# Kernel tuning notes

Hardware: AMD Instinct MI355X
Metric: run time of the kernel (lower is better)

## Reference

```python
import jax, jax.numpy as jnp
import numpy as np

HEAD_DIM = 16

def setup_inputs() -> dict:
    key = jax.random.key(0)
    ks = jax.random.split(key, 5)
    unif, h, d = 128, 8, 16
    batch, n = 4, 2048
    return {
        "Wq": jax.random.normal(ks[0], (unif, h, d), jnp.float32) * 0.05,
        "Wk": jax.random.normal(ks[1], (unif, h, d), jnp.float32) * 0.05,
        "Wv": jax.random.normal(ks[2], (unif, d, h), jnp.float32) * 0.05,
        "Wo": jax.random.normal(ks[3], (d, h, unif), jnp.float32) * 0.05,
        "vec": jax.random.normal(ks[4], (batch, n, unif), jnp.float32),
    }

def reference(Wq, Wk, Wv, Wo, vec):
    # projections: 'kij,abk->abij'
    qv = jnp.einsum('khd,bnk->bnhd', Wq, vec)          # [b,n,h,d]
    kv = jnp.einsum('khd,bnk->bnhd', Wk, vec)          # [b,n,h,d]
    vv = jnp.einsum('kdh,bnk->bndh', Wv, vec)          # [b,n,d,h]
    # full O(N^2) score tensor: 'aibk,ajbk->aijb'
    compat = jnp.einsum('bihd,bjhd->bijh', qv, kv) / np.sqrt(HEAD_DIM)  # [b,n,n,h]
    weight = jax.nn.softmax(compat, axis=2)
    # 'aijb,ajkb->aikb'
    received = jnp.einsum('bijh,bjdh->bidh', weight, vv)  # [b,n,d,h]
    # 'ijk,alij->alk'
    mha = jnp.einsum('dho,bndh->bno', Wo, received)       # [b,n,unif]
    return mha
```

## Files before the change

### kernel.cpp

```cpp
#include <hip/hip_runtime.h>
#include <hip/hip_bf16.h>

#define UNIF 128
#define NH   8
#define HD   16
#define BATCH 4
#define SEQ  2048
#define ROWS (BATCH*SEQ)

typedef __attribute__((ext_vector_type(8)))  short bf16x8;
typedef __attribute__((ext_vector_type(16))) float f32x16;
typedef __attribute__((ext_vector_type(4)))  float f32x4;
typedef __attribute__((ext_vector_type(4)))  unsigned uint32x4;
typedef __attribute__((ext_vector_type(2)))  unsigned uint2v;

static __device__ __forceinline__ unsigned f2bf(float x) {
    unsigned u = __builtin_bit_cast(unsigned, x);
    return (u + 0x7fffu + ((u >> 16) & 1u)) >> 16;
}
static __device__ __forceinline__ unsigned pkbf(float a, float b) {
    return f2bf(a) | (f2bf(b) << 16);
}
static __device__ __forceinline__ unsigned short bfs(float x) {
    return (unsigned short)f2bf(x);
}
static __device__ __forceinline__ unsigned cvtpk(float a, float b) {
    unsigned r;
    asm("v_cvt_pk_bf16_f32 %0, %1, %2" : "=v"(r) : "v"(a), "v"(b));
    return r;
}
static __device__ __forceinline__ void plswap(unsigned &a, unsigned &b) {
    uint2v r = __builtin_amdgcn_permlane32_swap(a, b, false, false);
    a = r[0]; b = r[1];
}
static __device__ __forceinline__ bf16x8 ld8f(const float* p) {
    const float4 x = *(const float4*)p;
    const float4 y = *(const float4*)(p + 4);
    uint32x4 u = { cvtpk(x.x, x.y), cvtpk(x.z, x.w),
                   cvtpk(y.x, y.y), cvtpk(y.z, y.w) };
    return __builtin_bit_cast(bf16x8, u);
}

__global__ __launch_bounds__(256) void prep_kernel(
    const float* __restrict__ Wq, const float* __restrict__ Wk,
    const float* __restrict__ Wv, const float* __restrict__ Wo,
    unsigned short* __restrict__ Wqt, unsigned short* __restrict__ Wkt,
    unsigned short* __restrict__ Wvt, unsigned short* __restrict__ Wot)
{
    const int m  = blockIdx.x >> 3;
    const int r0 = (blockIdx.x & 7) * 16;
    unsigned short* dst = (m==0)?Wqt:(m==1)?Wkt:(m==2)?Wvt:Wot;
    const float qsc = 0.25f * 1.4426950408889634f;
    for (int t = threadIdx.x; t < 16*UNIF; t += 256) {
        const int r = r0 + (t >> 7), s = t & 127;
        float val;
        if (m == 0)      val = Wq[s*UNIF + r] * qsc;
        else if (m == 1) val = Wk[s*UNIF + r];
        else if (m == 2) val = Wv[s*UNIF + (r & 15)*NH + (r >> 4)];
        else             val = Wo[((s & 15)*NH + (s >> 4))*UNIF + r];
        dst[r*UNIF + s] = bfs(val);
    }
}

__global__ __launch_bounds__(256) void proj_kernel(
    const float* __restrict__ vec,  const unsigned short* __restrict__ Wqt,
    const unsigned short* __restrict__ Wkt, const unsigned short* __restrict__ Wvt,
    unsigned short* __restrict__ Qbf, unsigned short* __restrict__ Kbf,
    unsigned short* __restrict__ Vt)
{
    const int sel  = blockIdx.y;
    const int row0 = blockIdx.x * 32;
    const int b    = row0 >> 11;
    const int n0   = row0 & (SEQ-1);
    const int lane = threadIdx.x & 63;
    const int w    = threadIdx.x >> 6;
    const int l15  = lane & 15, g = lane >> 4;
    const f32x4 Z4 = {0.f,0.f,0.f,0.f};

    if (sel < 2) {
        const unsigned short* Wt = sel ? Wkt : Wqt;
        unsigned short* dst = sel ? Kbf : Qbf;
        const int rw = row0 + (w & 1)*16;
        const int nb = rw & (SEQ-1);
        bf16x8 a[4];
        #pragma unroll
        for (int t = 0; t < 4; ++t)
            a[t] = ld8f(vec + (size_t)(rw + l15)*UNIF + 32*t + 8*g);
        const int c0 = (w >> 1) * 64;
        #pragma unroll
        for (int j = 0; j < 4; ++j) {
            const int ctile = c0 + 16*j;
            f32x4 acc = Z4;
            #pragma unroll
            for (int t = 0; t < 4; ++t) {
                const bf16x8 bfr = *(const bf16x8*)(Wt + (size_t)(ctile + l15)*UNIF + 32*t + 8*g);
                acc = __builtin_amdgcn_mfma_f32_16x16x32_bf16(a[t], bfr, acc, 0, 0, 0);
            }
            const int h = ctile >> 4;
            #pragma unroll
            for (int r = 0; r < 4; ++r)
                dst[((size_t)(b*NH + h)*SEQ + nb + 4*g + r)*HD + l15] = bfs(acc[r]);
        }
    } else {
        bf16x8 a[2][4], bb[2][4];
        #pragma unroll
        for (int j = 0; j < 2; ++j)
            #pragma unroll
            for (int t = 0; t < 4; ++t)
                a[j][t] = *(const bf16x8*)(Wvt + (size_t)(w*32 + 16*j + l15)*UNIF + 32*t + 8*g);
        #pragma unroll
        for (int u = 0; u < 2; ++u)
            #pragma unroll
            for (int t = 0; t < 4; ++t)
                bb[u][t] = ld8f(vec + (size_t)(row0 + 16*u + l15)*UNIF + 32*t + 8*g);
        #pragma unroll
        for (int j = 0; j < 2; ++j) {
            #pragma unroll
            for (int u = 0; u < 2; ++u) {
                f32x4 acc = Z4;
                #pragma unroll
                for (int t = 0; t < 4; ++t)
                    acc = __builtin_amdgcn_mfma_f32_16x16x32_bf16(a[j][t], bb[u][t], acc, 0, 0, 0);
                #pragma unroll
                for (int r = 0; r < 4; ++r) {
                    const int c = w*32 + 16*j + 4*g + r;
                    const int h = c >> 4, d = c & 15;
                    Vt[((size_t)(b*NH + h)*HD + d)*SEQ + n0 + 16*u + l15] = bfs(acc[r]);
                }
            }
        }
    }
}

__global__ __launch_bounds__(256, 3) void attn_kernel(
    const unsigned short* __restrict__ Qbf, const unsigned short* __restrict__ Kbf,
    const unsigned short* __restrict__ Vt, unsigned short* __restrict__ rb)
{
    __shared__ float Obuf[2][2][2][9][32];

    const int lane = threadIdx.x & 63;
    const int w    = threadIdx.x >> 6;
    const int bh   = blockIdx.y;
    const int i0   = blockIdx.x * 64;
    const int l31  = lane & 31, hi = lane >> 5;

    const bf16x8 qA = *(const bf16x8*)(Qbf + ((size_t)bh*SEQ + i0      + l31)*HD + 8*hi);
    const bf16x8 qC = *(const bf16x8*)(Qbf + ((size_t)bh*SEQ + i0 + 32 + l31)*HD + 8*hi);
    const unsigned short* kp   = Kbf + (size_t)bh*SEQ*HD + ((size_t)(w*(SEQ/4) + l31))*HD + 8*hi;
    const unsigned short* vrow = Vt  + ((size_t)bh*HD + l31)*SEQ + w*(SEQ/4);

    const unsigned ov = (l31 == 16 || l31 == 20) ? 0x3F803F80u : 0u;
    const uint32x4 ac4 = {ov, ov, ov, ov};
    const bf16x8 acst = __builtin_bit_cast(bf16x8, ac4);

    f32x16 OA = {0.f,0.f,0.f,0.f,0.f,0.f,0.f,0.f,0.f,0.f,0.f,0.f,0.f,0.f,0.f,0.f};
    f32x16 OC = OA;
    const f32x16 Zero = OA;

    auto process = [&](const bf16x8& qB, const bf16x8& kA,
                       const bf16x8& av0, const bf16x8& av1, f32x16& O) {
        f32x16 S = __builtin_amdgcn_mfma_f32_32x32x16_bf16(kA, qB, Zero, 0, 0, 0);
        unsigned W0[4], W1[4];
        #pragma unroll
        for (int c = 0; c < 4; ++c) {
            W0[c] = cvtpk(__builtin_amdgcn_exp2f(S[4*c+0]), __builtin_amdgcn_exp2f(S[4*c+1]));
            W1[c] = cvtpk(__builtin_amdgcn_exp2f(S[4*c+2]), __builtin_amdgcn_exp2f(S[4*c+3]));
        }
        plswap(W0[0], W0[1]);  plswap(W1[0], W1[1]);
        plswap(W0[2], W0[3]);  plswap(W1[2], W1[3]);
        const uint32x4 fa = {W0[0], W1[0], W0[1], W1[1]};
        const uint32x4 fb = {W0[2], W1[2], W0[3], W1[3]};
        O = __builtin_amdgcn_mfma_f32_32x32x16_bf16(av0, __builtin_bit_cast(bf16x8, fa), O, 0, 0, 0);
        O = __builtin_amdgcn_mfma_f32_32x32x16_bf16(av1, __builtin_bit_cast(bf16x8, fb), O, 0, 0, 0);
    };

    constexpr int NT = (SEQ/4)/32;
    #pragma unroll 1
    for (int t = 0; t < NT; ++t) {
        const bf16x8 kA = *(const bf16x8*)(kp + (size_t)t*32*HD);
        bf16x8 av0 = acst, av1 = acst;
        if (l31 < 16) {
            av0 = *(const bf16x8*)(vrow + t*32 + 8*hi);
            av1 = *(const bf16x8*)(vrow + t*32 + 16 + 8*hi);
        }
        process(qA, kA, av0, av1, OA);
        process(qC, kA, av0, av1, OC);
    }

    const int buf = w >> 1;
    if (w & 1) {
        #pragma unroll
        for (int r = 0; r < 9; ++r) {
            Obuf[0][buf][hi][r][l31] = OA[r];
            Obuf[1][buf][hi][r][l31] = OC[r];
        }
    }
    __syncthreads();
    if (!(w & 1)) {
        #pragma unroll
        for (int r = 0; r < 9; ++r) {
            OA[r] += Obuf[0][buf][hi][r][l31];
            OC[r] += Obuf[1][buf][hi][r][l31];
        }
        if (w == 2) {
            #pragma unroll
            for (int r = 0; r < 9; ++r) {
                Obuf[0][1][hi][r][l31] = OA[r];
                Obuf[1][1][hi][r][l31] = OC[r];
            }
        }
    }
    __syncthreads();
    if (w == 0) {
        #pragma unroll
        for (int r = 0; r < 9; ++r) {
            OA[r] += Obuf[0][1][hi][r][l31];
            OC[r] += Obuf[1][1][hi][r][l31];
        }
        const int b = bh >> 3, h = bh & 7;
        #pragma unroll
        for (int it = 0; it < 2; ++it) {
            const f32x16& O = it ? OC : OA;
            const float inv = 1.f / O[8];
            const unsigned a0 = pkbf(O[0]*inv, O[1]*inv);
            const unsigned a1 = pkbf(O[2]*inv, O[3]*inv);
            const unsigned a2 = pkbf(O[4]*inv, O[5]*inv);
            const unsigned a3 = pkbf(O[6]*inv, O[7]*inv);
            unsigned short* base = rb + ((size_t)b*SEQ + i0 + it*32 + l31)*UNIF + h*HD + hi*4;
            uint2 u01; u01.x = a0; u01.y = a1;
            uint2 u23; u23.x = a2; u23.y = a3;
            *(uint2*)(base)     = u01;
            *(uint2*)(base + 8) = u23;
        }
    }
}

__global__ __launch_bounds__(256) void out_kernel(
    const unsigned short* __restrict__ rb, const unsigned short* __restrict__ Wot,
    float* __restrict__ out)
{
    const int row0 = blockIdx.x * 32;
    const int lane = threadIdx.x & 63;
    const int w    = threadIdx.x >> 6;
    const int l15  = lane & 15, g = lane >> 4;
    const int rw   = row0 + (w & 1)*16;
    const int oc   = blockIdx.y*32 + (w >> 1)*16;
    const f32x4 Z4 = {0.f,0.f,0.f,0.f};

    bf16x8 a[4];
    #pragma unroll
    for (int t = 0; t < 4; ++t)
        a[t] = *(const bf16x8*)(rb + (size_t)(rw + l15)*UNIF + 32*t + 8*g);

    f32x4 acc = Z4;
    #pragma unroll
    for (int t = 0; t < 4; ++t) {
        const bf16x8 bfr = *(const bf16x8*)(Wot + (size_t)(oc + l15)*UNIF + 32*t + 8*g);
        acc = __builtin_amdgcn_mfma_f32_16x16x32_bf16(a[t], bfr, acc, 0, 0, 0);
    }
    #pragma unroll
    for (int r = 0; r < 4; ++r)
        out[(size_t)(rw + 4*g + r)*UNIF + oc + l15] = acc[r];
}

extern "C" void kernel_launch(void* const* d_in, const int* in_sizes, int n_in,
                              void* d_out, int out_size, void* d_ws, size_t ws_size,
                              hipStream_t stream) {
    const float* Wq  = (const float*)d_in[0];
    const float* Wk  = (const float*)d_in[1];
    const float* Wv  = (const float*)d_in[2];
    const float* Wo  = (const float*)d_in[3];
    const float* vec = (const float*)d_in[4];
    float* out = (float*)d_out;

    const size_t tsz = (size_t)BATCH*NH*SEQ*HD;
    unsigned short* Wqt = (unsigned short*)d_ws;
    unsigned short* Wkt = Wqt + UNIF*UNIF;
    unsigned short* Wvt = Wkt + UNIF*UNIF;
    unsigned short* Wot = Wvt + UNIF*UNIF;
    unsigned short* Qbf = Wot + UNIF*UNIF;
    unsigned short* Kbf = Qbf + tsz;
    unsigned short* Vt  = Kbf + tsz;
    unsigned short* rb  = Vt  + tsz;

    prep_kernel<<<32, 256, 0, stream>>>(Wq, Wk, Wv, Wo, Wqt, Wkt, Wvt, Wot);
    proj_kernel<<<dim3(ROWS/32, 3), 256, 0, stream>>>(vec, Wqt, Wkt, Wvt, Qbf, Kbf, Vt);
    attn_kernel<<<dim3(SEQ/64, BATCH*NH), 256, 0, stream>>>(Qbf, Kbf, Vt, rb);
    out_kernel<<<dim3(ROWS/32, 4), 256, 0, stream>>>(rb, Wot, out);
}
```

Baseline: 49.36 us.

## Merge projection passes, widen output tiles, stage weights in LDS, add MFMA priority hints

The projection kernel now loads each 32-row tile of vec once and computes Q, K and V in a single pass, where before it ran three separate grid slices that each reread vec. The output kernel gives each block all 128 output columns, so the rb tile is read once. The weight-prep kernel uses 4 blocks that each stage a whole weight matrix in LDS and then transpose it, replacing 32 blocks doing strided global reads. The attention kernel wraps its MFMA calls in s_setprio hints. In exchange, the projection and output kernels launch fewer, larger blocks, and prep runs on only 4 blocks.

```diff
diff --git a/kernel.cpp b/kernel.cpp
--- a/kernel.cpp
+++ b/kernel.cpp
@@ -47,17 +47,26 @@
     unsigned short* __restrict__ Wqt, unsigned short* __restrict__ Wkt,
     unsigned short* __restrict__ Wvt, unsigned short* __restrict__ Wot)
 {
-    const int m  = blockIdx.x >> 3;
-    const int r0 = (blockIdx.x & 7) * 16;
+    __shared__ float L[UNIF][UNIF + 1];
+    const int m = blockIdx.x;
+    const float* src = (m==0)?Wq:(m==1)?Wk:(m==2)?Wv:Wo;
     unsigned short* dst = (m==0)?Wqt:(m==1)?Wkt:(m==2)?Wvt:Wot;
     const float qsc = 0.25f * 1.4426950408889634f;
-    for (int t = threadIdx.x; t < 16*UNIF; t += 256) {
-        const int r = r0 + (t >> 7), s = t & 127;
+
+    for (int t = threadIdx.x; t < UNIF*UNIF/4; t += 256) {
+        const float4 v = ((const float4*)src)[t];
+        const int row = t >> 5, col = (t & 31) * 4;
+        L[row][col] = v.x; L[row][col+1] = v.y; L[row][col+2] = v.z; L[row][col+3] = v.w;
+    }
+    __syncthreads();
+
+    for (int t = threadIdx.x; t < UNIF*UNIF; t += 256) {
+        const int r = t >> 7, s = t & 127;
         float val;
-        if (m == 0)      val = Wq[s*UNIF + r] * qsc;
-        else if (m == 1) val = Wk[s*UNIF + r];
-        else if (m == 2) val = Wv[s*UNIF + (r & 15)*NH + (r >> 4)];
-        else             val = Wo[((s & 15)*NH + (s >> 4))*UNIF + r];
+        if (m == 0)      val = L[s][r] * qsc;
+        else if (m == 1) val = L[s][r];
+        else if (m == 2) val = L[s][(r & 15)*NH + (r >> 4)];
+        else             val = L[(s & 15)*NH + (s >> 4)][r];
         dst[r*UNIF + s] = bfs(val);
     }
 }
@@ -68,65 +77,60 @@
     unsigned short* __restrict__ Qbf, unsigned short* __restrict__ Kbf,
     unsigned short* __restrict__ Vt)
 {
-    const int sel  = blockIdx.y;
     const int row0 = blockIdx.x * 32;
     const int b    = row0 >> 11;
     const int n0   = row0 & (SEQ-1);
     const int lane = threadIdx.x & 63;
     const int w    = threadIdx.x >> 6;
     const int l15  = lane & 15, g = lane >> 4;
+    const int rh   = w & 1, ch = w >> 1;
     const f32x4 Z4 = {0.f,0.f,0.f,0.f};
 
-    if (sel < 2) {
-        const unsigned short* Wt = sel ? Wkt : Wqt;
-        unsigned short* dst = sel ? Kbf : Qbf;
-        const int rw = row0 + (w & 1)*16;
-        const int nb = rw & (SEQ-1);
-        bf16x8 a[4];
+    bf16x8 a[2][4];
+    #pragma unroll
+    for (int u = 0; u < 2; ++u)
         #pragma unroll
         for (int t = 0; t < 4; ++t)
-            a[t] = ld8f(vec + (size_t)(rw + l15)*UNIF + 32*t + 8*g);
-        const int c0 = (w >> 1) * 64;
+            a[u][t] = ld8f(vec + (size_t)(row0 + 16*u + l15)*UNIF + 32*t + 8*g);
+
+    #pragma unroll
+    for (int mqk = 0; mqk < 2; ++mqk) {
+        const unsigned short* Wt = mqk ? Wkt : Wqt;
+        unsigned short* dst = mqk ? Kbf : Qbf;
         #pragma unroll
         for (int j = 0; j < 4; ++j) {
-            const int ctile = c0 + 16*j;
+            const int ctile = ch*64 + 16*j;
             f32x4 acc = Z4;
             #pragma unroll
             for (int t = 0; t < 4; ++t) {
                 const bf16x8 bfr = *(const bf16x8*)(Wt + (size_t)(ctile + l15)*UNIF + 32*t + 8*g);
-                acc = __builtin_amdgcn_mfma_f32_16x16x32_bf16(a[t], bfr, acc, 0, 0, 0);
+                acc = __builtin_amdgcn_mfma_f32_16x16x32_bf16(a[rh][t], bfr, acc, 0, 0, 0);
             }
             const int h = ctile >> 4;
             #pragma unroll
             for (int r = 0; r < 4; ++r)
-                dst[((size_t)(b*NH + h)*SEQ + nb + 4*g + r)*HD + l15] = bfs(acc[r]);
-        }
-    } else {
-        bf16x8 a[2][4], bb[2][4];
-        #pragma unroll
-        for (int j = 0; j < 2; ++j)
+                dst[((size_t)(b*NH + h)*SEQ + n0 + rh*16 + 4*g + r)*HD + l15] = bfs(acc[r]);
+        }
+    }
+
+    #pragma unroll
+    for (int jj = 0; jj < 2; ++jj) {
+        const int c0 = w*32 + 16*jj;
+        bf16x8 av[4];
+        #pragma unroll
+        for (int t = 0; t < 4; ++t)
+            av[t] = *(const bf16x8*)(Wvt + (size_t)(c0 + l15)*UNIF + 32*t + 8*g);
+        #pragma unroll
+        for (int u = 0; u < 2; ++u) {
+            f32x4 acc = Z4;
             #pragma unroll
             for (int t = 0; t < 4; ++t)
-                a[j][t] = *(const bf16x8*)(Wvt + (size_t)(w*32 + 16*j + l15)*UNIF + 32*t + 8*g);
-        #pragma unroll
-        for (int u = 0; u < 2; ++u)
-            #pragma unroll
-            for (int t = 0; t < 4; ++t)
-                bb[u][t] = ld8f(vec + (size_t)(row0 + 16*u + l15)*UNIF + 32*t + 8*g);
-        #pragma unroll
-        for (int j = 0; j < 2; ++j) {
-            #pragma unroll
-            for (int u = 0; u < 2; ++u) {
-                f32x4 acc = Z4;
-                #pragma unroll
-                for (int t = 0; t < 4; ++t)
-                    acc = __builtin_amdgcn_mfma_f32_16x16x32_bf16(a[j][t], bb[u][t], acc, 0, 0, 0);
-                #pragma unroll
-                for (int r = 0; r < 4; ++r) {
-                    const int c = w*32 + 16*j + 4*g + r;
-                    const int h = c >> 4, d = c & 15;
-                    Vt[((size_t)(b*NH + h)*HD + d)*SEQ + n0 + 16*u + l15] = bfs(acc[r]);
-                }
+                acc = __builtin_amdgcn_mfma_f32_16x16x32_bf16(av[t], a[u][t], acc, 0, 0, 0);
+            #pragma unroll
+            for (int r = 0; r < 4; ++r) {
+                const int c = c0 + 4*g + r;
+                const int h = c >> 4, d = c & 15;
+                Vt[((size_t)(b*NH + h)*HD + d)*SEQ + n0 + 16*u + l15] = bfs(acc[r]);
             }
         }
     }
@@ -159,7 +163,9 @@
 
     auto process = [&](const bf16x8& qB, const bf16x8& kA,
                        const bf16x8& av0, const bf16x8& av1, f32x16& O) {
+        __builtin_amdgcn_s_setprio(1);
         f32x16 S = __builtin_amdgcn_mfma_f32_32x32x16_bf16(kA, qB, Zero, 0, 0, 0);
+        __builtin_amdgcn_s_setprio(0);
         unsigned W0[4], W1[4];
         #pragma unroll
         for (int c = 0; c < 4; ++c) {
@@ -170,8 +176,10 @@
         plswap(W0[2], W0[3]);  plswap(W1[2], W1[3]);
         const uint32x4 fa = {W0[0], W1[0], W0[1], W1[1]};
         const uint32x4 fb = {W0[2], W1[2], W0[3], W1[3]};
+        __builtin_amdgcn_s_setprio(1);
         O = __builtin_amdgcn_mfma_f32_32x32x16_bf16(av0, __builtin_bit_cast(bf16x8, fa), O, 0, 0, 0);
         O = __builtin_amdgcn_mfma_f32_32x32x16_bf16(av1, __builtin_bit_cast(bf16x8, fb), O, 0, 0, 0);
+        __builtin_amdgcn_s_setprio(0);
     };
 
     constexpr int NT = (SEQ/4)/32;
@@ -244,7 +252,7 @@
     const int w    = threadIdx.x >> 6;
     const int l15  = lane & 15, g = lane >> 4;
     const int rw   = row0 + (w & 1)*16;
-    const int oc   = blockIdx.y*32 + (w >> 1)*16;
+    const int oc0  = (w >> 1)*64;
     const f32x4 Z4 = {0.f,0.f,0.f,0.f};
 
     bf16x8 a[4];
@@ -252,15 +260,19 @@
     for (int t = 0; t < 4; ++t)
         a[t] = *(const bf16x8*)(rb + (size_t)(rw + l15)*UNIF + 32*t + 8*g);
 
-    f32x4 acc = Z4;
-    #pragma unroll
-    for (int t = 0; t < 4; ++t) {
-        const bf16x8 bfr = *(const bf16x8*)(Wot + (size_t)(oc + l15)*UNIF + 32*t + 8*g);
-        acc = __builtin_amdgcn_mfma_f32_16x16x32_bf16(a[t], bfr, acc, 0, 0, 0);
-    }
-    #pragma unroll
-    for (int r = 0; r < 4; ++r)
-        out[(size_t)(rw + 4*g + r)*UNIF + oc + l15] = acc[r];
+    #pragma unroll
+    for (int j = 0; j < 4; ++j) {
+        const int oc = oc0 + 16*j;
+        f32x4 acc = Z4;
+        #pragma unroll
+        for (int t = 0; t < 4; ++t) {
+            const bf16x8 bfr = *(const bf16x8*)(Wot + (size_t)(oc + l15)*UNIF + 32*t + 8*g);
+            acc = __builtin_amdgcn_mfma_f32_16x16x32_bf16(a[t], bfr, acc, 0, 0, 0);
+        }
+        #pragma unroll
+        for (int r = 0; r < 4; ++r)
+            out[(size_t)(rw + 4*g + r)*UNIF + oc + l15] = acc[r];
+    }
 }
 
 extern "C" void kernel_launch(void* const* d_in, const int* in_sizes, int n_in,
@@ -283,8 +295,8 @@
     unsigned short* Vt  = Kbf + tsz;
     unsigned short* rb  = Vt  + tsz;
 
-    prep_kernel<<<32, 256, 0, stream>>>(Wq, Wk, Wv, Wo, Wqt, Wkt, Wvt, Wot);
-    proj_kernel<<<dim3(ROWS/32, 3), 256, 0, stream>>>(vec, Wqt, Wkt, Wvt, Qbf, Kbf, Vt);
+    prep_kernel<<<4, 256, 0, stream>>>(Wq, Wk, Wv, Wo, Wqt, Wkt, Wvt, Wot);
+    proj_kernel<<<ROWS/32, 256, 0, stream>>>(vec, Wqt, Wkt, Wvt, Qbf, Kbf, Vt);
     attn_kernel<<<dim3(SEQ/64, BATCH*NH), 256, 0, stream>>>(Qbf, Kbf, Vt, rb);
-    out_kernel<<<dim3(ROWS/32, 4), 256, 0, stream>>>(rb, Wot, out);
-}
+    out_kernel<<<ROWS/32, 256, 0, stream>>>(rb, Wot, out);
+}
```

New measurement: 68.69 us. 1.39x slower.
